# Performance work log

Measured on AMD Instinct MI355X. Metric: run time of the kernel, lower is better.

The kernel has to match this reference:

```python
import jax, jax.numpy as jnp
import numpy as np

EMBED_DIM = 1024
NUM_HEADS = 16
HEAD_DIM = EMBED_DIM // NUM_HEADS


def layer_norm(x, gamma, beta, eps=1e-5):
    mu = jnp.mean(x, axis=-1, keepdims=True)
    var = jnp.var(x, axis=-1, keepdims=True)
    return (x - mu) * jax.lax.rsqrt(var + eps) * gamma + beta


def setup_inputs() -> dict:
    key = jax.random.key(0)
    ks = jax.random.split(key, 8)
    D = EMBED_DIM
    s = 1.0 / np.sqrt(D)
    x = jax.random.normal(ks[0], (2, 2048, D), dtype=jnp.float32)
    Wq = jax.random.uniform(ks[1], (D, D), jnp.float32, -s, s)
    Wk = jax.random.uniform(ks[2], (D, D), jnp.float32, -s, s)
    Wv = jax.random.uniform(ks[3], (D, D), jnp.float32, -s, s)
    W1 = jax.random.uniform(ks[4], (D, 4 * D), jnp.float32, -s, s)
    b1 = jnp.zeros((4 * D,), jnp.float32)
    W2 = jax.random.uniform(ks[5], (4 * D, D), jnp.float32, -1.0 / np.sqrt(4 * D), 1.0 / np.sqrt(4 * D))
    b2 = jnp.zeros((D,), jnp.float32)
    g1 = jnp.ones((D,), jnp.float32); be1 = jnp.zeros((D,), jnp.float32)
    g2 = jnp.ones((D,), jnp.float32); be2 = jnp.zeros((D,), jnp.float32)
    return {"x": x, "Wq": Wq, "Wk": Wk, "Wv": Wv, "W1": W1, "b1": b1,
            "W2": W2, "b2": b2, "g1": g1, "be1": be1, "g2": g2, "be2": be2}


def reference(x, Wq, Wk, Wv, W1, b1, W2, b2, g1, be1, g2, be2):
    B, S, D = x.shape
    H, Hd = NUM_HEADS, HEAD_DIM
    x_norm = layer_norm(x, g1, be1)
    # QKV projections (no bias), split into heads: [B, H, S, Hd]
    q = (x_norm @ Wq).reshape(B, S, H, Hd).transpose(0, 2, 1, 3)
    k = (x_norm @ Wk).reshape(B, S, H, Hd).transpose(0, 2, 1, 3)
    v = (x_norm @ Wv).reshape(B, S, H, Hd).transpose(0, 2, 1, 3)
    energy = jnp.einsum('bhqd,bhkd->bhqk', q, k)
    attn = jax.nn.softmax(energy / jnp.sqrt(jnp.float32(Hd)), axis=-1)
    out = jnp.einsum('bhqk,bhkd->bhqd', attn, v)
    attention = out.transpose(0, 2, 1, 3).reshape(B, S, D)
    x_res = attention + x
    x_norm2 = layer_norm(x_res, g2, be2)
    # Faithful quirk: FFN applied to x_res (not x_norm2)
    ffn_out = jax.nn.relu(x_res @ W1 + b1) @ W2 + b2
    return ffn_out + x_norm2
```

## Files before the change

### kernel.cpp

```cpp
#include <hip/hip_runtime.h>
#include <hip/hip_bf16.h>
#include <stdint.h>

typedef __hip_bfloat16 bf16;
typedef __attribute__((ext_vector_type(4))) float f32x4;
typedef __attribute__((ext_vector_type(8))) short s16x8;
typedef __attribute__((ext_vector_type(4))) short s16x4;

#define DEV static __device__ __forceinline__

DEV short f2bf(float f) {
  bf16 h = __float2bfloat16(f);
  short s;
  __builtin_memcpy(&s, &h, 2);
  return s;
}
DEV float bf2f(short s) {
  bf16 h;
  __builtin_memcpy(&h, &s, 2);
  return __bfloat162float(h);
}

__global__ __launch_bounds__(256) void transpose_cvt(
    const float* __restrict__ W, bf16* __restrict__ Wt, int K, int N)
{
  __shared__ float tile[32][33];
  const int n0 = blockIdx.x << 5;
  const int k0 = blockIdx.y << 5;
  const int tx = threadIdx.x & 31, ty = threadIdx.x >> 5;
#pragma unroll
  for (int i = 0; i < 4; ++i)
    tile[ty + i * 8][tx] = W[(size_t)(k0 + ty + i * 8) * N + n0 + tx];
  __syncthreads();
#pragma unroll
  for (int i = 0; i < 4; ++i)
    Wt[(size_t)(n0 + ty + i * 8) * K + k0 + tx] = __float2bfloat16(tile[tx][ty + i * 8]);
}

__global__ __launch_bounds__(256) void ln_bf16(
    const float* __restrict__ x, const float* __restrict__ g,
    const float* __restrict__ be, bf16* __restrict__ out)
{
  const int t = threadIdx.x;
  const size_t row = blockIdx.x;
  const float4 v = ((const float4*)(x + row * 1024))[t];
  float s = v.x + v.y + v.z + v.w;
  float ss = v.x * v.x + v.y * v.y + v.z * v.z + v.w * v.w;
#pragma unroll
  for (int off = 32; off > 0; off >>= 1) {
    s += __shfl_down(s, off);
    ss += __shfl_down(ss, off);
  }
  __shared__ float sh[8];
  const int wave = t >> 6, lane = t & 63;
  if (!lane) { sh[wave] = s; sh[4 + wave] = ss; }
  __syncthreads();
  s = sh[0] + sh[1] + sh[2] + sh[3];
  ss = sh[4] + sh[5] + sh[6] + sh[7];
  const float mean = s * (1.f / 1024.f);
  const float rstd = rsqrtf(ss * (1.f / 1024.f) - mean * mean + 1e-5f);
  const float4 gv = ((const float4*)g)[t];
  const float4 bv = ((const float4*)be)[t];
  s16x4 o;
  o[0] = f2bf((v.x - mean) * rstd * gv.x + bv.x);
  o[1] = f2bf((v.y - mean) * rstd * gv.y + bv.y);
  o[2] = f2bf((v.z - mean) * rstd * gv.z + bv.z);
  o[3] = f2bf((v.w - mean) * rstd * gv.w + bv.w);
  ((s16x4*)(out + row * 1024))[t] = o;
}

__global__ __launch_bounds__(256) void add_ln_bf16(
    const float* __restrict__ a, const float* __restrict__ x,
    const float* __restrict__ g, const float* __restrict__ be,
    bf16* __restrict__ xres, bf16* __restrict__ xnorm)
{
  const int t = threadIdx.x;
  const size_t row = blockIdx.x;
  const float4 av = ((const float4*)(a + row * 1024))[t];
  const float4 xv = ((const float4*)(x + row * 1024))[t];
  float4 v;
  v.x = av.x + xv.x; v.y = av.y + xv.y; v.z = av.z + xv.z; v.w = av.w + xv.w;
  float s = v.x + v.y + v.z + v.w;
  float ss = v.x * v.x + v.y * v.y + v.z * v.z + v.w * v.w;
#pragma unroll
  for (int off = 32; off > 0; off >>= 1) {
    s += __shfl_down(s, off);
    ss += __shfl_down(ss, off);
  }
  __shared__ float sh[8];
  const int wave = t >> 6, lane = t & 63;
  if (!lane) { sh[wave] = s; sh[4 + wave] = ss; }
  __syncthreads();
  s = sh[0] + sh[1] + sh[2] + sh[3];
  ss = sh[4] + sh[5] + sh[6] + sh[7];
  const float mean = s * (1.f / 1024.f);
  const float rstd = rsqrtf(ss * (1.f / 1024.f) - mean * mean + 1e-5f);
  const float4 gv = ((const float4*)g)[t];
  const float4 bv = ((const float4*)be)[t];
  s16x4 r, o;
  r[0] = f2bf(v.x); r[1] = f2bf(v.y); r[2] = f2bf(v.z); r[3] = f2bf(v.w);
  o[0] = f2bf((v.x - mean) * rstd * gv.x + bv.x);
  o[1] = f2bf((v.y - mean) * rstd * gv.y + bv.y);
  o[2] = f2bf((v.z - mean) * rstd * gv.z + bv.z);
  o[3] = f2bf((v.w - mean) * rstd * gv.w + bv.w);
  ((s16x4*)(xres + row * 1024))[t] = r;
  ((s16x4*)(xnorm + row * 1024))[t] = o;
}

template <int EPI>
__global__ __launch_bounds__(256) void gemm_bt(
    const bf16* __restrict__ A, const bf16* __restrict__ Bt,
    void* __restrict__ C, const float* __restrict__ bias,
    const bf16* __restrict__ add_bf16, int M, int N, int K)
{
  __shared__ bf16 sA[128 * 64];
  __shared__ bf16 sB[128 * 64];
  const int tid = threadIdx.x;
  const int wave = tid >> 6, lane = tid & 63;
  const int fr = lane & 15, fg = lane >> 4;
  const int f7 = fr & 7;
  const int wr = wave >> 1, wc = wave & 1;
  const int nbx = N >> 7;
  int bid = blockIdx.x;
  if ((gridDim.x & 7) == 0) {
    const int cpx = gridDim.x >> 3;
    bid = (bid & 7) * cpx + (bid >> 3);
  }
  const int brow = (bid / nbx) << 7;
  const int bcol = (bid % nbx) << 7;

  f32x4 acc[4][4] = {};

  const int rsub = lane >> 3;
  const int cl = (lane & 7) ^ rsub;
  size_t ga[4], gb[4];
  int la[4];
#pragma unroll
  for (int j = 0; j < 4; ++j) {
    const int r = wave * 32 + j * 8;
    ga[j] = (size_t)(brow + r + rsub) * K + cl * 8;
    gb[j] = (size_t)(bcol + r + rsub) * K + cl * 8;
    la[j] = r * 64;
  }

  for (int kt = 0; kt < K; kt += 64) {
#pragma unroll
    for (int j = 0; j < 4; ++j) {
      __builtin_amdgcn_global_load_lds(
          (const __attribute__((address_space(1))) uint32_t*)(A + ga[j] + kt),
          (__attribute__((address_space(3))) uint32_t*)(&sA[la[j]]), 16, 0, 0);
      __builtin_amdgcn_global_load_lds(
          (const __attribute__((address_space(1))) uint32_t*)(Bt + gb[j] + kt),
          (__attribute__((address_space(3))) uint32_t*)(&sB[la[j]]), 16, 0, 0);
    }
    __syncthreads();

    s16x8 af[4][2], bfr[4][2];
#pragma unroll
    for (int m = 0; m < 4; ++m)
#pragma unroll
      for (int kk = 0; kk < 2; ++kk)
        af[m][kk] = *(const s16x8*)(&sA[(wr * 64 + m * 16 + fr) * 64 +
                                        (((kk * 4 + fg) ^ f7) << 3)]);
#pragma unroll
    for (int n = 0; n < 4; ++n)
#pragma unroll
      for (int kk = 0; kk < 2; ++kk)
        bfr[n][kk] = *(const s16x8*)(&sB[(wc * 64 + n * 16 + fr) * 64 +
                                         (((kk * 4 + fg) ^ f7) << 3)]);
#pragma unroll
    for (int kk = 0; kk < 2; ++kk)
#pragma unroll
      for (int m = 0; m < 4; ++m)
#pragma unroll
        for (int n = 0; n < 4; ++n)
          acc[m][n] = __builtin_amdgcn_mfma_f32_16x16x32_bf16(
              af[m][kk], bfr[n][kk], acc[m][n], 0, 0, 0);
    __syncthreads();
  }

  const int crow = brow + wr * 64;
  const int ccol = bcol + wc * 64;
#pragma unroll
  for (int m = 0; m < 4; ++m) {
#pragma unroll
    for (int n = 0; n < 4; ++n) {
      const int col = ccol + n * 16 + fr;
#pragma unroll
      for (int j = 0; j < 4; ++j) {
        const int row = crow + m * 16 + fg * 4 + j;
        float v = acc[m][n][j];
        if (EPI == 0) {
          ((bf16*)C)[(size_t)row * N + col] = __float2bfloat16(v);
        } else if (EPI == 1) {
          v += bias[col];
          v = fmaxf(v, 0.f);
          ((bf16*)C)[(size_t)row * N + col] = __float2bfloat16(v);
        } else {
          float a;
          {
            bf16 hb = add_bf16[(size_t)row * N + col];
            a = __bfloat162float(hb);
          }
          ((float*)C)[(size_t)row * N + col] = v + bias[col] + a;
        }
      }
    }
  }
}

__global__ __launch_bounds__(512, 4) void attn_fwd(
    const bf16* __restrict__ QK, const bf16* __restrict__ Vt,
    float* __restrict__ Out)
{
  const int LDK = 2048;
  const int qt = blockIdx.x;
  const int bh = blockIdx.y;
  const int b = bh >> 4, h = bh & 15;
  const int tid = threadIdx.x;
  const int wave = tid >> 6, lane = tid & 63;
  const int fr = lane & 15, fg = lane >> 4;
  const int f7 = fr & 7;

  const short* base = (const short*)QK + (size_t)b * 2048 * LDK;
  const short* Qp = base + h * 64;
  const short* Kp = base + 1024 + h * 64;
  const short* Vp = (const short*)Vt + (size_t)h * 64 * 4096 + b * 2048;
  const int q0 = qt * 128 + wave * 16;

  __shared__ short Kbuf[2][64 * 64];
  __shared__ short Vbuf[2][64 * 64];
  __shared__ short P_lds[8][16 * 72];
  short* Pw = P_lds[wave];

  const int rsub = lane >> 3;
  const int clog = (lane & 7) ^ rsub;
  const short* Ksrc = Kp + (size_t)(8 * wave + rsub) * LDK + clog * 8;
  const short* Vsrc = Vp + (size_t)(8 * wave + rsub) * 4096 + clog * 8;

  s16x8 qf0 = *(const s16x8*)(Qp + (size_t)(q0 + fr) * LDK + fg * 8);
  s16x8 qf1 = *(const s16x8*)(Qp + (size_t)(q0 + fr) * LDK + 32 + fg * 8);
#pragma unroll
  for (int i = 0; i < 8; ++i) {
    qf0[i] = f2bf(bf2f(qf0[i]) * 0.125f);
    qf1[i] = f2bf(bf2f(qf1[i]) * 0.125f);
  }

  f32x4 acc[4] = {};
  f32x4 mrow = {-1e30f, -1e30f, -1e30f, -1e30f};
  f32x4 lrow = {};

#define STAGE(bi, kt)                                                          \
  do {                                                                         \
    __builtin_amdgcn_global_load_lds(                                          \
        (const __attribute__((address_space(1))) uint32_t*)(Ksrc + (size_t)(kt) * LDK), \
        (__attribute__((address_space(3))) uint32_t*)(&Kbuf[bi][wave * 512]),  \
        16, 0, 0);                                                             \
    __builtin_amdgcn_global_load_lds(                                          \
        (const __attribute__((address_space(1))) uint32_t*)(Vsrc + (kt)),      \
        (__attribute__((address_space(3))) uint32_t*)(&Vbuf[bi][wave * 512]),  \
        16, 0, 0);                                                             \
  } while (0)

  int cur = 0;
  STAGE(0, 0);

  for (int kt = 0; kt < 2048; kt += 64) {
    if (kt + 64 < 2048) {
      STAGE(cur ^ 1, kt + 64);
      asm volatile("s_waitcnt vmcnt(2)" ::: "memory");
    } else {
      asm volatile("s_waitcnt vmcnt(0)" ::: "memory");
    }
    __builtin_amdgcn_s_barrier();
    __builtin_amdgcn_sched_barrier(0);

    const short* Kb = Kbuf[cur];
    const short* Vb = Vbuf[cur];

    f32x4 e[4];
#pragma unroll
    for (int t = 0; t < 4; ++t) {
      const int ro = (t * 16 + fr) * 64;
      const s16x8 k0 = *(const s16x8*)(Kb + ro + ((fg ^ f7) << 3));
      const s16x8 k1 = *(const s16x8*)(Kb + ro + (((4 + fg) ^ f7) << 3));
      f32x4 z = {};
      z = __builtin_amdgcn_mfma_f32_16x16x32_bf16(qf0, k0, z, 0, 0, 0);
      z = __builtin_amdgcn_mfma_f32_16x16x32_bf16(qf1, k1, z, 0, 0, 0);
      e[t] = z;
    }

    f32x4 lmx;
#pragma unroll
    for (int j = 0; j < 4; ++j)
      lmx[j] = fmaxf(fmaxf(e[0][j], e[1][j]), fmaxf(e[2][j], e[3][j]));
    const bool need = (lmx[0] > mrow[0] + 8.f) | (lmx[1] > mrow[1] + 8.f) |
                      (lmx[2] > mrow[2] + 8.f) | (lmx[3] > mrow[3] + 8.f);
    if (__any(need)) {
      f32x4 mx = lmx;
#pragma unroll
      for (int d = 1; d < 16; d <<= 1)
#pragma unroll
        for (int j = 0; j < 4; ++j) mx[j] = fmaxf(mx[j], __shfl_xor(mx[j], d));
#pragma unroll
      for (int j = 0; j < 4; ++j) {
        const float mn = fmaxf(mrow[j], mx[j]);
        const float al = __expf(mrow[j] - mn);
        lrow[j] *= al;
        mrow[j] = mn;
#pragma unroll
        for (int nn = 0; nn < 4; ++nn) acc[nn][j] *= al;
      }
    }

#pragma unroll
    for (int j = 0; j < 4; ++j) {
#pragma unroll
      for (int t = 0; t < 4; ++t) e[t][j] = __expf(e[t][j] - mrow[j]);
      lrow[j] += (e[0][j] + e[1][j]) + (e[2][j] + e[3][j]);
    }

#pragma unroll
    for (int t = 0; t < 4; ++t)
#pragma unroll
      for (int j = 0; j < 4; ++j)
        Pw[(fg * 4 + j) * 72 + t * 16 + fr] = f2bf(e[t][j]);
    const s16x8 pf0 = *(const s16x8*)(Pw + fr * 72 + fg * 8);
    const s16x8 pf1 = *(const s16x8*)(Pw + fr * 72 + 32 + fg * 8);

#pragma unroll
    for (int nn = 0; nn < 4; ++nn) {
      const int ro = (nn * 16 + fr) * 64;
      const s16x8 vf0 = *(const s16x8*)(Vb + ro + ((fg ^ f7) << 3));
      const s16x8 vf1 = *(const s16x8*)(Vb + ro + (((4 + fg) ^ f7) << 3));
      acc[nn] = __builtin_amdgcn_mfma_f32_16x16x32_bf16(pf0, vf0, acc[nn], 0, 0, 0);
      acc[nn] = __builtin_amdgcn_mfma_f32_16x16x32_bf16(pf1, vf1, acc[nn], 0, 0, 0);
    }

    __builtin_amdgcn_s_barrier();
    __builtin_amdgcn_sched_barrier(0);
    cur ^= 1;
  }
#undef STAGE

#pragma unroll
  for (int d = 1; d < 16; d <<= 1)
#pragma unroll
    for (int j = 0; j < 4; ++j) lrow[j] += __shfl_xor(lrow[j], d);
  f32x4 inv;
#pragma unroll
  for (int j = 0; j < 4; ++j) inv[j] = 1.0f / lrow[j];
  float* outp = Out + (size_t)(b * 2048 + q0) * 1024 + h * 64;
#pragma unroll
  for (int nn = 0; nn < 4; ++nn)
#pragma unroll
    for (int j = 0; j < 4; ++j)
      outp[(size_t)(fg * 4 + j) * 1024 + nn * 16 + fr] = acc[nn][j] * inv[j];
}

extern "C" void kernel_launch(void* const* d_in, const int* in_sizes, int n_in,
                              void* d_out, int out_size, void* d_ws, size_t ws_size,
                              hipStream_t stream)
{
  const float* x   = (const float*)d_in[0];
  const float* Wq  = (const float*)d_in[1];
  const float* Wk  = (const float*)d_in[2];
  const float* Wv  = (const float*)d_in[3];
  const float* W1  = (const float*)d_in[4];
  const float* b1  = (const float*)d_in[5];
  const float* W2  = (const float*)d_in[6];
  const float* b2  = (const float*)d_in[7];
  const float* g1  = (const float*)d_in[8];
  const float* be1 = (const float*)d_in[9];
  const float* g2  = (const float*)d_in[10];
  const float* be2 = (const float*)d_in[11];
  float* out = (float*)d_out;

  const int M = 4096, D = 1024, DF = 4096;

  bf16* Wqk_t = (bf16*)d_ws;
  bf16* Wv_t  = Wqk_t + (size_t)2048 * 1024;
  bf16* W1t   = Wv_t + (size_t)1024 * 1024;
  bf16* W2t   = W1t + (size_t)4096 * 1024;
  bf16* big   = W2t + (size_t)4096 * 1024;
  bf16* QK    = big;
  bf16* Vt    = big + (size_t)8 * 1024 * 1024;
  bf16* hbuf  = big;
  char* p2    = (char*)(big + (size_t)16 * 1024 * 1024);
  bf16* xnorm = (bf16*)p2;
  float* attnO = (float*)p2;
  char* p3    = p2 + (size_t)M * D * sizeof(float);
  bf16* xres  = (bf16*)p3;
  bf16* xnorm2 = xres + (size_t)M * D;

  transpose_cvt<<<dim3(32, 32), 256, 0, stream>>>(Wq, Wqk_t, D, D);
  transpose_cvt<<<dim3(32, 32), 256, 0, stream>>>(Wk, Wqk_t + (size_t)D * D, D, D);
  transpose_cvt<<<dim3(32, 32), 256, 0, stream>>>(Wv, Wv_t, D, D);
  transpose_cvt<<<dim3(128, 32), 256, 0, stream>>>(W1, W1t, D, DF);
  transpose_cvt<<<dim3(32, 128), 256, 0, stream>>>(W2, W2t, DF, D);
  ln_bf16<<<M, 256, 0, stream>>>(x, g1, be1, xnorm);
  gemm_bt<0><<<(M / 128) * (2048 / 128), 256, 0, stream>>>(
      xnorm, Wqk_t, QK, nullptr, nullptr, M, 2048, D);
  gemm_bt<0><<<(D / 128) * (M / 128), 256, 0, stream>>>(
      Wv_t, xnorm, Vt, nullptr, nullptr, D, M, D);
  attn_fwd<<<dim3(16, 32), 512, 0, stream>>>(QK, Vt, attnO);
  add_ln_bf16<<<M, 256, 0, stream>>>(attnO, x, g2, be2, xres, xnorm2);
  gemm_bt<1><<<(M / 128) * (DF / 128), 256, 0, stream>>>(
      xres, W1t, hbuf, b1, nullptr, M, DF, D);
  gemm_bt<2><<<(M / 128) * (D / 128), 256, 0, stream>>>(
      hbuf, W2t, out, b2, xnorm2, M, D, DF);
}
```

Measured before the change: 273.2 us.

## Double-buffer LDS tiles in GEMM to overlap global loads with MFMA

Adds a second pair of shared-memory tile buffers to the GEMM and prefetches the next K tile via global_load_lds while computing on the current one. This cuts the per-iteration barrier count from two to one and is meant to hide global memory latency behind MFMA work. It doubles LDS usage per block, which may reduce occupancy.

```diff
diff --git a/kernel.cpp b/kernel.cpp
--- a/kernel.cpp
+++ b/kernel.cpp
@@ -113,8 +113,10 @@
     void* __restrict__ C, const float* __restrict__ bias,
     const bf16* __restrict__ add_bf16, int M, int N, int K)
 {
-  __shared__ bf16 sA[128 * 64];
-  __shared__ bf16 sB[128 * 64];
+  __shared__ bf16 sA0[128 * 64];
+  __shared__ bf16 sB0[128 * 64];
+  __shared__ bf16 sA1[128 * 64];
+  __shared__ bf16 sB1[128 * 64];
   const int tid = threadIdx.x;
   const int wave = tid >> 6, lane = tid & 63;
   const int fr = lane & 15, fg = lane >> 4;
@@ -143,41 +145,70 @@
     la[j] = r * 64;
   }
 
-  for (int kt = 0; kt < K; kt += 64) {
-#pragma unroll
-    for (int j = 0; j < 4; ++j) {
-      __builtin_amdgcn_global_load_lds(
-          (const __attribute__((address_space(1))) uint32_t*)(A + ga[j] + kt),
-          (__attribute__((address_space(3))) uint32_t*)(&sA[la[j]]), 16, 0, 0);
-      __builtin_amdgcn_global_load_lds(
-          (const __attribute__((address_space(1))) uint32_t*)(Bt + gb[j] + kt),
-          (__attribute__((address_space(3))) uint32_t*)(&sB[la[j]]), 16, 0, 0);
-    }
-    __syncthreads();
-
-    s16x8 af[4][2], bfr[4][2];
-#pragma unroll
-    for (int m = 0; m < 4; ++m)
-#pragma unroll
-      for (int kk = 0; kk < 2; ++kk)
-        af[m][kk] = *(const s16x8*)(&sA[(wr * 64 + m * 16 + fr) * 64 +
-                                        (((kk * 4 + fg) ^ f7) << 3)]);
-#pragma unroll
-    for (int n = 0; n < 4; ++n)
-#pragma unroll
-      for (int kk = 0; kk < 2; ++kk)
-        bfr[n][kk] = *(const s16x8*)(&sB[(wc * 64 + n * 16 + fr) * 64 +
-                                         (((kk * 4 + fg) ^ f7) << 3)]);
-#pragma unroll
-    for (int kk = 0; kk < 2; ++kk)
-#pragma unroll
-      for (int m = 0; m < 4; ++m)
-#pragma unroll
-        for (int n = 0; n < 4; ++n)
-          acc[m][n] = __builtin_amdgcn_mfma_f32_16x16x32_bf16(
-              af[m][kk], bfr[n][kk], acc[m][n], 0, 0, 0);
-    __syncthreads();
-  }
+#define GSTAGE(SA, SB, kt)                                                     \
+  do {                                                                         \
+    _Pragma("unroll")                                                          \
+    for (int j = 0; j < 4; ++j) {                                              \
+      __builtin_amdgcn_global_load_lds(                                        \
+          (const __attribute__((address_space(1))) uint32_t*)(A + ga[j] + (kt)), \
+          (__attribute__((address_space(3))) uint32_t*)(&SA[la[j]]), 16, 0, 0);  \
+      __builtin_amdgcn_global_load_lds(                                        \
+          (const __attribute__((address_space(1))) uint32_t*)(Bt + gb[j] + (kt)),\
+          (__attribute__((address_space(3))) uint32_t*)(&SB[la[j]]), 16, 0, 0);  \
+    }                                                                          \
+  } while (0)
+
+#define COMPUTE(SA, SB)                                                        \
+  do {                                                                         \
+    s16x8 af[4][2], bfr[4][2];                                                 \
+    _Pragma("unroll")                                                          \
+    for (int m = 0; m < 4; ++m)                                                \
+      _Pragma("unroll")                                                        \
+      for (int kk = 0; kk < 2; ++kk)                                           \
+        af[m][kk] = *(const s16x8*)(&SA[(wr * 64 + m * 16 + fr) * 64 +         \
+                                        (((kk * 4 + fg) ^ f7) << 3)]);         \
+    _Pragma("unroll")                                                          \
+    for (int n = 0; n < 4; ++n)                                                \
+      _Pragma("unroll")                                                        \
+      for (int kk = 0; kk < 2; ++kk)                                           \
+        bfr[n][kk] = *(const s16x8*)(&SB[(wc * 64 + n * 16 + fr) * 64 +        \
+                                         (((kk * 4 + fg) ^ f7) << 3)]);        \
+    _Pragma("unroll")                                                          \
+    for (int kk = 0; kk < 2; ++kk)                                             \
+      _Pragma("unroll")                                                        \
+      for (int m = 0; m < 4; ++m)                                              \
+        _Pragma("unroll")                                                      \
+        for (int n = 0; n < 4; ++n)                                            \
+          acc[m][n] = __builtin_amdgcn_mfma_f32_16x16x32_bf16(                 \
+              af[m][kk], bfr[n][kk], acc[m][n], 0, 0, 0);                      \
+  } while (0)
+
+  GSTAGE(sA0, sB0, 0);
+  __syncthreads();
+
+  int kt = 0;
+  for (;;) {
+    if (kt + 64 < K) {
+      GSTAGE(sA1, sB1, kt + 64);
+      COMPUTE(sA0, sB0);
+      __syncthreads();
+    } else {
+      COMPUTE(sA0, sB0);
+      break;
+    }
+    kt += 64;
+    if (kt + 64 < K) {
+      GSTAGE(sA0, sB0, kt + 64);
+      COMPUTE(sA1, sB1);
+      __syncthreads();
+    } else {
+      COMPUTE(sA1, sB1);
+      break;
+    }
+    kt += 64;
+  }
+#undef GSTAGE
+#undef COMPUTE
 
   const int crow = brow + wr * 64;
   const int ccol = bcol + wc * 64;
```

Result: faster. 248.0 us (-9.2%).
